# Optimization experiments

Hardware: AMD Instinct MI355X
Metric: run time of the kernel (lower is better)

## Reference

```python
import jax, jax.numpy as jnp
import numpy as np


def setup_inputs() -> dict:
    key = jax.random.key(0)
    k_in, k_w, k_b = jax.random.split(key, 3)
    B, S, H, HEADS = 16, 4096, 768, 8
    inputs = jax.random.normal(k_in, (B, S, H), dtype=jnp.float32)
    # xavier_uniform for Linear(H -> HEADS): limit = sqrt(6/(fan_in+fan_out))
    limit = float(np.sqrt(6.0 / (H + HEADS)))
    W = jax.random.uniform(k_w, (HEADS, H), dtype=jnp.float32, minval=-limit, maxval=limit)
    b = jnp.zeros((HEADS,), dtype=jnp.float32)  # nn.Linear default bias init left as zeros-equivalent scale; use uniform per torch default
    bound = float(1.0 / np.sqrt(H))
    b = jax.random.uniform(k_b, (HEADS,), dtype=jnp.float32, minval=-bound, maxval=bound)
    return {"inputs": inputs, "W": W, "b": b}


def reference(inputs, W, b):
    # atten = Linear(inputs) -> [B, S, heads]; transpose -> [B, heads, S]
    atten = jnp.einsum("bsh,eh->bes", inputs, W) + b[None, :, None]  # [B, heads, S]
    atten_sm = jax.nn.softmax(atten, axis=-1)                        # softmax over seq
    out = jnp.einsum("bes,bsh->beh", atten_sm, inputs)               # [B, heads, H]
    return (out, atten)
```

## Files before the change

### kernel.cpp

```cpp
#include <hip/hip_runtime.h>
#include <hip/hip_bf16.h>
#include <math.h>

constexpr int Bn = 16;
constexpr int Sn = 4096;
constexpr int Hn = 768;
constexpr int En = 8;
constexpr int OUT_N = Bn * En * Hn;
constexpr int NBLK  = 512;
constexpr int NSC   = 32;

__global__ __launch_bounds__(256, 2) void k_fused(
    const float* __restrict__ x, const float* __restrict__ W,
    const float* __restrict__ bias, float* __restrict__ att,
    float* __restrict__ part, float* __restrict__ sumexpG) {
  const int lane = threadIdx.x & 63;
  const int w    = threadIdx.x >> 6;
  const int wid  = blockIdx.x * 4 + w;
  const int b    = wid >> 7;
  const int wl   = wid & 127;

  float4 wf[8][3];
#pragma unroll
  for (int e = 0; e < 8; ++e)
#pragma unroll
    for (int j = 0; j < 3; ++j)
      wf[e][j] = *(const float4*)(W + e * 768 + (lane << 2) + (j << 8));
  const float bv = bias[lane & 7];

  float4 acc[8][3];
#pragma unroll
  for (int e = 0; e < 8; ++e)
#pragma unroll
    for (int j = 0; j < 3; ++j) acc[e][j] = make_float4(0.f, 0.f, 0.f, 0.f);
  float sume = 0.0f;

  int r = b * Sn + wl;
  const float4* rp = (const float4*)(x + (size_t)r * Hn);
  float4 c0 = rp[lane], c1 = rp[lane + 64], c2 = rp[lane + 128];

  for (int t = 0; t < 32; ++t) {
    const bool more = (t + 1 < 32);
    float4 n0, n1, n2;
    if (more) {
      const float4* np_ = (const float4*)(x + (size_t)(r + 128) * Hn);
      n0 = np_[lane]; n1 = np_[lane + 64]; n2 = np_[lane + 128];
    }

    float a8[8];
#pragma unroll
    for (int e = 0; e < 8; ++e) {
      float a = c0.x * wf[e][0].x;
      a = fmaf(c0.y, wf[e][0].y, a);
      a = fmaf(c0.z, wf[e][0].z, a);
      a = fmaf(c0.w, wf[e][0].w, a);
      a = fmaf(c1.x, wf[e][1].x, a);
      a = fmaf(c1.y, wf[e][1].y, a);
      a = fmaf(c1.z, wf[e][1].z, a);
      a = fmaf(c1.w, wf[e][1].w, a);
      a = fmaf(c2.x, wf[e][2].x, a);
      a = fmaf(c2.y, wf[e][2].y, a);
      a = fmaf(c2.z, wf[e][2].z, a);
      a = fmaf(c2.w, wf[e][2].w, a);
      a8[e] = a;
    }

    float v4[4];
#pragma unroll
    for (int k = 0; k < 4; ++k) {
      const float pa = a8[2 * k], pb = a8[2 * k + 1];
      const bool hi = (lane & 1);
      const float send = hi ? pa : pb;
      const float keep = hi ? pb : pa;
      v4[k] = keep + __shfl_xor(send, 1, 64);
    }
    float v2[2];
#pragma unroll
    for (int k = 0; k < 2; ++k) {
      const float pa = v4[2 * k], pb = v4[2 * k + 1];
      const bool hi = (lane & 2);
      const float send = hi ? pa : pb;
      const float keep = hi ? pb : pa;
      v2[k] = keep + __shfl_xor(send, 2, 64);
    }
    float u;
    {
      const float pa = v2[0], pb = v2[1];
      const bool hi = (lane & 4);
      const float send = hi ? pa : pb;
      const float keep = hi ? pb : pa;
      u = keep + __shfl_xor(send, 4, 64);
    }
    u += __shfl_xor(u, 8, 64);
    u += __shfl_xor(u, 16, 64);
    u += __shfl_xor(u, 32, 64);

    const float logit = u + bv;
    if (lane < 8)
      att[(size_t)((b << 3) + lane) * Sn + (r & 4095)] = logit;

    const float texp = __expf(logit);
    sume += texp;

#pragma unroll
    for (int e = 0; e < 8; ++e) {
      const float we = __shfl(texp, e, 64);
      acc[e][0].x = fmaf(we, c0.x, acc[e][0].x);
      acc[e][0].y = fmaf(we, c0.y, acc[e][0].y);
      acc[e][0].z = fmaf(we, c0.z, acc[e][0].z);
      acc[e][0].w = fmaf(we, c0.w, acc[e][0].w);
      acc[e][1].x = fmaf(we, c1.x, acc[e][1].x);
      acc[e][1].y = fmaf(we, c1.y, acc[e][1].y);
      acc[e][1].z = fmaf(we, c1.z, acc[e][1].z);
      acc[e][1].w = fmaf(we, c1.w, acc[e][1].w);
      acc[e][2].x = fmaf(we, c2.x, acc[e][2].x);
      acc[e][2].y = fmaf(we, c2.y, acc[e][2].y);
      acc[e][2].z = fmaf(we, c2.z, acc[e][2].z);
      acc[e][2].w = fmaf(we, c2.w, acc[e][2].w);
    }

    if (!more) break;
    r += 128;
    c0 = n0; c1 = n1; c2 = n2;
  }

  __shared__ float4 lacc[3 * 24 * 64];
  __shared__ float  lsum[32];
  if (w > 0) {
    float4* dst = &lacc[(w - 1) * 24 * 64];
#pragma unroll
    for (int e = 0; e < 8; ++e)
#pragma unroll
      for (int j = 0; j < 3; ++j)
        dst[(e * 3 + j) * 64 + lane] = acc[e][j];
  }
  if (lane < 8) lsum[w * 8 + lane] = sume;
  __syncthreads();

  if (w == 0) {
#pragma unroll
    for (int g = 0; g < 3; ++g) {
      const float4* src = &lacc[g * 24 * 64];
#pragma unroll
      for (int e = 0; e < 8; ++e)
#pragma unroll
        for (int j = 0; j < 3; ++j) {
          const float4 v = src[(e * 3 + j) * 64 + lane];
          acc[e][j].x += v.x; acc[e][j].y += v.y;
          acc[e][j].z += v.z; acc[e][j].w += v.w;
        }
    }
    float4* po = (float4*)(part + (size_t)blockIdx.x * (En * Hn));
#pragma unroll
    for (int e = 0; e < 8; ++e)
#pragma unroll
      for (int j = 0; j < 3; ++j)
        po[e * 192 + j * 64 + lane] = acc[e][j];
    if (lane < 8)
      sumexpG[blockIdx.x * 8 + lane] =
          lsum[lane] + lsum[8 + lane] + lsum[16 + lane] + lsum[24 + lane];
  }
}

__global__ __launch_bounds__(256) void k_final(const float* __restrict__ part,
                                               const float* __restrict__ sumexpG,
                                               float* __restrict__ out) {
  __shared__ float Zs[128];
  const int t = threadIdx.x;
  if (t < 128) {
    const int b = t >> 3, e = t & 7;
    float z = 0.0f;
    for (int c = 0; c < NSC; ++c) z += sumexpG[((b * NSC + c) << 3) + e];
    Zs[t] = 1.0f / z;
  }
  __syncthreads();

  const int o4 = blockIdx.x * 256 + t;
  const int b  = o4 / 1536;
  const int r4 = o4 - b * 1536;
  const int e  = r4 / 192;
  const float4* p4 = (const float4*)part + (size_t)(b * NSC) * 1536 + r4;
  float4 a = make_float4(0.f, 0.f, 0.f, 0.f);
  for (int c = 0; c < NSC; ++c) {
    const float4 v = p4[(size_t)c * 1536];
    a.x += v.x; a.y += v.y; a.z += v.z; a.w += v.w;
  }
  const float inv = Zs[(b << 3) + e];
  a.x *= inv; a.y *= inv; a.z *= inv; a.w *= inv;
  ((float4*)out)[o4] = a;
}

extern "C" void kernel_launch(void* const* d_in, const int* in_sizes, int n_in,
                              void* d_out, int out_size, void* d_ws, size_t ws_size,
                              hipStream_t stream) {
  const float* x    = (const float*)d_in[0];
  const float* W    = (const float*)d_in[1];
  const float* bias = (const float*)d_in[2];
  float* out = (float*)d_out;
  float* att = out + OUT_N;
  float* part    = (float*)d_ws;
  float* sumexpG = part + NBLK * En * Hn;

  k_fused<<<NBLK, 256, 0, stream>>>(x, W, bias, att, part, sumexpG);
  k_final<<<OUT_N / 4 / 256, 256, 0, stream>>>(part, sumexpG, out);
}
```

Before: 286.1 us.

## Split heads across wave pairs and quadruple block count for occupancy

New measurement: 300.1 us. 1.05x slower.

```diff
diff --git a/kernel.cpp b/kernel.cpp
--- a/kernel.cpp
+++ b/kernel.cpp
@@ -7,104 +7,98 @@
 constexpr int Hn = 768;
 constexpr int En = 8;
 constexpr int OUT_N = Bn * En * Hn;
-constexpr int NBLK  = 512;
-constexpr int NSC   = 32;
+constexpr int NBLK  = 2048;
+constexpr int NSC   = 128;
 
-__global__ __launch_bounds__(256, 2) void k_fused(
+__global__ __launch_bounds__(256, 3) void k_fused(
     const float* __restrict__ x, const float* __restrict__ W,
     const float* __restrict__ bias, float* __restrict__ att,
     float* __restrict__ part, float* __restrict__ sumexpG) {
   const int lane = threadIdx.x & 63;
   const int w    = threadIdx.x >> 6;
-  const int wid  = blockIdx.x * 4 + w;
-  const int b    = wid >> 7;
-  const int wl   = wid & 127;
+  const int half = w & 1;
+  const int grp  = w >> 1;
+  const int bid  = blockIdx.x;
+  const int b    = bid >> 7;
+  const int sc   = bid & 127;
 
-  float4 wf[8][3];
+  float4 wf[4][3];
 #pragma unroll
-  for (int e = 0; e < 8; ++e)
+  for (int e = 0; e < 4; ++e)
 #pragma unroll
     for (int j = 0; j < 3; ++j)
-      wf[e][j] = *(const float4*)(W + e * 768 + (lane << 2) + (j << 8));
-  const float bv = bias[lane & 7];
+      wf[e][j] = *(const float4*)(W + (half * 4 + e) * 768 + (lane << 2) + (j << 8));
+  const float bv = bias[half * 4 + (lane & 3)];
 
-  float4 acc[8][3];
+  float4 acc[4][3];
 #pragma unroll
-  for (int e = 0; e < 8; ++e)
+  for (int e = 0; e < 4; ++e)
 #pragma unroll
     for (int j = 0; j < 3; ++j) acc[e][j] = make_float4(0.f, 0.f, 0.f, 0.f);
   float sume = 0.0f;
 
-  int r = b * Sn + wl;
-  const float4* rp = (const float4*)(x + (size_t)r * Hn);
+  const int s0 = sc * 32 + grp * 16;
+  const float* xb = x + (size_t)b * Sn * Hn;
+
+  const float4* rp = (const float4*)(xb + (size_t)s0 * Hn);
   float4 c0 = rp[lane], c1 = rp[lane + 64], c2 = rp[lane + 128];
 
-  for (int t = 0; t < 32; ++t) {
-    const bool more = (t + 1 < 32);
+  for (int t = 0; t < 16; ++t) {
+    const bool more = (t + 1 < 16);
     float4 n0, n1, n2;
     if (more) {
-      const float4* np_ = (const float4*)(x + (size_t)(r + 128) * Hn);
+      const float4* np_ = (const float4*)(xb + (size_t)(s0 + t + 1) * Hn);
       n0 = np_[lane]; n1 = np_[lane + 64]; n2 = np_[lane + 128];
     }
 
-    float a8[8];
+    float a4[4];
 #pragma unroll
-    for (int e = 0; e < 8; ++e) {
-      float a = c0.x * wf[e][0].x;
-      a = fmaf(c0.y, wf[e][0].y, a);
-      a = fmaf(c0.z, wf[e][0].z, a);
-      a = fmaf(c0.w, wf[e][0].w, a);
-      a = fmaf(c1.x, wf[e][1].x, a);
-      a = fmaf(c1.y, wf[e][1].y, a);
-      a = fmaf(c1.z, wf[e][1].z, a);
-      a = fmaf(c1.w, wf[e][1].w, a);
-      a = fmaf(c2.x, wf[e][2].x, a);
-      a = fmaf(c2.y, wf[e][2].y, a);
-      a = fmaf(c2.z, wf[e][2].z, a);
-      a = fmaf(c2.w, wf[e][2].w, a);
-      a8[e] = a;
+    for (int e = 0; e < 4; ++e) {
+      float pe = fmaf(c0.z, wf[e][0].z, c0.x * wf[e][0].x);
+      float po = fmaf(c0.w, wf[e][0].w, c0.y * wf[e][0].y);
+      pe = fmaf(c1.x, wf[e][1].x, pe);
+      po = fmaf(c1.y, wf[e][1].y, po);
+      pe = fmaf(c1.z, wf[e][1].z, pe);
+      po = fmaf(c1.w, wf[e][1].w, po);
+      pe = fmaf(c2.x, wf[e][2].x, pe);
+      po = fmaf(c2.y, wf[e][2].y, po);
+      pe = fmaf(c2.z, wf[e][2].z, pe);
+      po = fmaf(c2.w, wf[e][2].w, po);
+      a4[e] = pe + po;
     }
 
-    float v4[4];
+    float v2[2];
 #pragma unroll
-    for (int k = 0; k < 4; ++k) {
-      const float pa = a8[2 * k], pb = a8[2 * k + 1];
+    for (int k = 0; k < 2; ++k) {
+      const float pa = a4[2 * k], pb = a4[2 * k + 1];
       const bool hi = (lane & 1);
       const float send = hi ? pa : pb;
       const float keep = hi ? pb : pa;
-      v4[k] = keep + __shfl_xor(send, 1, 64);
-    }
-    float v2[2];
-#pragma unroll
-    for (int k = 0; k < 2; ++k) {
-      const float pa = v4[2 * k], pb = v4[2 * k + 1];
-      const bool hi = (lane & 2);
-      const float send = hi ? pa : pb;
-      const float keep = hi ? pb : pa;
-      v2[k] = keep + __shfl_xor(send, 2, 64);
+      v2[k] = keep + __shfl_xor(send, 1, 64);
     }
     float u;
     {
       const float pa = v2[0], pb = v2[1];
-      const bool hi = (lane & 4);
+      const bool hi = (lane & 2);
       const float send = hi ? pa : pb;
       const float keep = hi ? pb : pa;
-      u = keep + __shfl_xor(send, 4, 64);
+      u = keep + __shfl_xor(send, 2, 64);
     }
+    u += __shfl_xor(u, 4, 64);
     u += __shfl_xor(u, 8, 64);
     u += __shfl_xor(u, 16, 64);
     u += __shfl_xor(u, 32, 64);
 
     const float logit = u + bv;
-    if (lane < 8)
-      att[(size_t)((b << 3) + lane) * Sn + (r & 4095)] = logit;
+    if (lane < 4)
+      att[(size_t)((b << 3) + half * 4 + lane) * Sn + (s0 + t)] = logit;
 
     const float texp = __expf(logit);
     sume += texp;
 
 #pragma unroll
-    for (int e = 0; e < 8; ++e) {
-      const float we = __shfl(texp, e, 64);
+    for (int e = 0; e < 4; ++e) {
+      const float we = __shfl(texp, e, 4);
       acc[e][0].x = fmaf(we, c0.x, acc[e][0].x);
       acc[e][0].y = fmaf(we, c0.y, acc[e][0].y);
       acc[e][0].z = fmaf(we, c0.z, acc[e][0].z);
@@ -120,45 +114,39 @@
     }
 
     if (!more) break;
-    r += 128;
     c0 = n0; c1 = n1; c2 = n2;
   }
 
-  __shared__ float4 lacc[3 * 24 * 64];
-  __shared__ float  lsum[32];
-  if (w > 0) {
-    float4* dst = &lacc[(w - 1) * 24 * 64];
+  __shared__ float4 lacc[2][12][64];
+  __shared__ float  lsum[4][4];
+  if (grp == 1) {
 #pragma unroll
-    for (int e = 0; e < 8; ++e)
+    for (int e = 0; e < 4; ++e)
 #pragma unroll
       for (int j = 0; j < 3; ++j)
-        dst[(e * 3 + j) * 64 + lane] = acc[e][j];
+        lacc[half][e * 3 + j][lane] = acc[e][j];
   }
-  if (lane < 8) lsum[w * 8 + lane] = sume;
+  if (lane < 4) lsum[w][lane] = sume;
   __syncthreads();
 
-  if (w == 0) {
+  if (grp == 0) {
 #pragma unroll
-    for (int g = 0; g < 3; ++g) {
-      const float4* src = &lacc[g * 24 * 64];
+    for (int e = 0; e < 4; ++e)
 #pragma unroll
-      for (int e = 0; e < 8; ++e)
+      for (int j = 0; j < 3; ++j) {
+        const float4 v = lacc[half][e * 3 + j][lane];
+        acc[e][j].x += v.x; acc[e][j].y += v.y;
+        acc[e][j].z += v.z; acc[e][j].w += v.w;
+      }
+    float4* po = (float4*)(part + (size_t)bid * (En * Hn));
 #pragma unroll
-        for (int j = 0; j < 3; ++j) {
-          const float4 v = src[(e * 3 + j) * 64 + lane];
-          acc[e][j].x += v.x; acc[e][j].y += v.y;
-          acc[e][j].z += v.z; acc[e][j].w += v.w;
-        }
-    }
-    float4* po = (float4*)(part + (size_t)blockIdx.x * (En * Hn));
-#pragma unroll
-    for (int e = 0; e < 8; ++e)
+    for (int e = 0; e < 4; ++e)
 #pragma unroll
       for (int j = 0; j < 3; ++j)
-        po[e * 192 + j * 64 + lane] = acc[e][j];
-    if (lane < 8)
-      sumexpG[blockIdx.x * 8 + lane] =
-          lsum[lane] + lsum[8 + lane] + lsum[16 + lane] + lsum[24 + lane];
+        po[(half * 4 + e) * 192 + j * 64 + lane] = acc[e][j];
+    if (lane < 4)
+      sumexpG[bid * 8 + half * 4 + lane] =
+          lsum[half][lane] + lsum[2 + half][lane];
   }
 }
 
@@ -199,7 +187,7 @@
   float* out = (float*)d_out;
   float* att = out + OUT_N;
   float* part    = (float*)d_ws;
-  float* sumexpG = part + NBLK * En * Hn;
+  float* sumexpG = part + (size_t)NBLK * En * Hn;
 
   k_fused<<<NBLK, 256, 0, stream>>>(x, W, bias, att, part, sumexpG);
   k_final<<<OUT_N / 4 / 256, 256, 0, stream>>>(part, sumexpG, out);
```

## Give each wave contiguous rows and store block partials in bf16

Applied to the files above, without the earlier changes.

Result: no change. 287.0 us (+0.3%).

```diff
diff --git a/kernel.cpp b/kernel.cpp
--- a/kernel.cpp
+++ b/kernel.cpp
@@ -10,15 +10,23 @@
 constexpr int NBLK  = 512;
 constexpr int NSC   = 32;
 
+__device__ __forceinline__ unsigned short f2bf(float f) {
+  const unsigned int u = __float_as_uint(f);
+  return (unsigned short)((u + 0x7FFFu + ((u >> 16) & 1u)) >> 16);
+}
+__device__ __forceinline__ float bf2f(unsigned short h) {
+  return __uint_as_float((unsigned int)h << 16);
+}
+
 __global__ __launch_bounds__(256, 2) void k_fused(
     const float* __restrict__ x, const float* __restrict__ W,
     const float* __restrict__ bias, float* __restrict__ att,
-    float* __restrict__ part, float* __restrict__ sumexpG) {
+    unsigned short* __restrict__ part, float* __restrict__ sumexpG) {
   const int lane = threadIdx.x & 63;
   const int w    = threadIdx.x >> 6;
-  const int wid  = blockIdx.x * 4 + w;
-  const int b    = wid >> 7;
-  const int wl   = wid & 127;
+  const int bid  = blockIdx.x;
+  const int b    = bid >> 5;
+  const int chunk = bid & 31;
 
   float4 wf[8][3];
 #pragma unroll
@@ -35,15 +43,16 @@
     for (int j = 0; j < 3; ++j) acc[e][j] = make_float4(0.f, 0.f, 0.f, 0.f);
   float sume = 0.0f;
 
-  int r = b * Sn + wl;
-  const float4* rp = (const float4*)(x + (size_t)r * Hn);
+  const int s0 = chunk * 128 + w * 32;
+  const float* xb = x + (size_t)b * Sn * Hn;
+  const float4* rp = (const float4*)(xb + (size_t)s0 * Hn);
   float4 c0 = rp[lane], c1 = rp[lane + 64], c2 = rp[lane + 128];
 
   for (int t = 0; t < 32; ++t) {
     const bool more = (t + 1 < 32);
     float4 n0, n1, n2;
     if (more) {
-      const float4* np_ = (const float4*)(x + (size_t)(r + 128) * Hn);
+      const float4* np_ = (const float4*)(xb + (size_t)(s0 + t + 1) * Hn);
       n0 = np_[lane]; n1 = np_[lane + 64]; n2 = np_[lane + 128];
     }
 
@@ -97,7 +106,7 @@
 
     const float logit = u + bv;
     if (lane < 8)
-      att[(size_t)((b << 3) + lane) * Sn + (r & 4095)] = logit;
+      att[(size_t)((b << 3) + lane) * Sn + (s0 + t)] = logit;
 
     const float texp = __expf(logit);
     sume += texp;
@@ -120,7 +129,6 @@
     }
 
     if (!more) break;
-    r += 128;
     c0 = n0; c1 = n1; c2 = n2;
   }
 
@@ -150,21 +158,27 @@
           acc[e][j].z += v.z; acc[e][j].w += v.w;
         }
     }
-    float4* po = (float4*)(part + (size_t)blockIdx.x * (En * Hn));
+    ushort4* po = (ushort4*)(part + (size_t)bid * (En * Hn));
 #pragma unroll
     for (int e = 0; e < 8; ++e)
 #pragma unroll
-      for (int j = 0; j < 3; ++j)
-        po[e * 192 + j * 64 + lane] = acc[e][j];
+      for (int j = 0; j < 3; ++j) {
+        ushort4 h;
+        h.x = f2bf(acc[e][j].x);
+        h.y = f2bf(acc[e][j].y);
+        h.z = f2bf(acc[e][j].z);
+        h.w = f2bf(acc[e][j].w);
+        po[e * 192 + j * 64 + lane] = h;
+      }
     if (lane < 8)
-      sumexpG[blockIdx.x * 8 + lane] =
+      sumexpG[bid * 8 + lane] =
           lsum[lane] + lsum[8 + lane] + lsum[16 + lane] + lsum[24 + lane];
   }
 }
 
-__global__ __launch_bounds__(256) void k_final(const float* __restrict__ part,
-                                               const float* __restrict__ sumexpG,
-                                               float* __restrict__ out) {
+__global__ __launch_bounds__(256) void k_final(
+    const unsigned short* __restrict__ part,
+    const float* __restrict__ sumexpG, float* __restrict__ out) {
   __shared__ float Zs[128];
   const int t = threadIdx.x;
   if (t < 128) {
@@ -179,11 +193,12 @@
   const int b  = o4 / 1536;
   const int r4 = o4 - b * 1536;
   const int e  = r4 / 192;
-  const float4* p4 = (const float4*)part + (size_t)(b * NSC) * 1536 + r4;
+  const ushort4* p4 =
+      (const ushort4*)part + (size_t)(b * NSC) * 1536 + r4;
   float4 a = make_float4(0.f, 0.f, 0.f, 0.f);
   for (int c = 0; c < NSC; ++c) {
-    const float4 v = p4[(size_t)c * 1536];
-    a.x += v.x; a.y += v.y; a.z += v.z; a.w += v.w;
+    const ushort4 h = p4[(size_t)c * 1536];
+    a.x += bf2f(h.x); a.y += bf2f(h.y); a.z += bf2f(h.z); a.w += bf2f(h.w);
   }
   const float inv = Zs[(b << 3) + e];
   a.x *= inv; a.y *= inv; a.z *= inv; a.w *= inv;
@@ -198,8 +213,8 @@
   const float* bias = (const float*)d_in[2];
   float* out = (float*)d_out;
   float* att = out + OUT_N;
-  float* part    = (float*)d_ws;
-  float* sumexpG = part + NBLK * En * Hn;
+  unsigned short* part = (unsigned short*)d_ws;
+  float* sumexpG = (float*)(part + (size_t)NBLK * En * Hn);
 
   k_fused<<<NBLK, 256, 0, stream>>>(x, W, bias, att, part, sumexpG);
   k_final<<<OUT_N / 4 / 256, 256, 0, stream>>>(part, sumexpG, out);
```
